# Kernel optimization log

Hardware: AMD Instinct MI355X
Metric: run time of the kernel (lower is better)

## Reference

```python
import jax, jax.numpy as jnp
import numpy as np

C, H_HEADS, L_LEV, M_PTS = 256, 4, 3, 4
TAU0 = 1.0


def _ln(x, g, b, eps=1e-5):
    mu = x.mean(-1, keepdims=True)
    var = ((x - mu) ** 2).mean(-1, keepdims=True)
    return (x - mu) * jax.lax.rsqrt(var + eps) * g + b


def _grid_sample(v, grid):
    """Bilinear grid_sample, padding_mode='zeros', align_corners=True.
    v: [B,C,Hin,Win], grid: [B,N,2] (x,y) in [-1,1] -> [B,N,C]"""
    B, Cc, Hin, Win = v.shape
    x = (grid[..., 0] + 1.0) * 0.5 * (Win - 1)
    y = (grid[..., 1] + 1.0) * 0.5 * (Hin - 1)
    x0 = jnp.floor(x); y0 = jnp.floor(y)
    wx1 = x - x0; wy1 = y - y0
    x0i = x0.astype(jnp.int32); y0i = y0.astype(jnp.int32)
    vflat = v.reshape(B, Cc, Hin * Win).transpose(0, 2, 1)  # [B,HW,C]

    def tap(yi, xi, w):
        valid = ((xi >= 0) & (xi < Win) & (yi >= 0) & (yi < Hin)).astype(v.dtype)
        idx = jnp.clip(yi, 0, Hin - 1) * Win + jnp.clip(xi, 0, Win - 1)  # [B,N]
        g = jax.vmap(lambda vf, i: vf[i])(vflat, idx)  # [B,N,C]
        return g * (w * valid)[..., None]

    return (tap(y0i, x0i, (1 - wy1) * (1 - wx1))
            + tap(y0i, x0i + 1, (1 - wy1) * wx1)
            + tap(y0i + 1, x0i, wy1 * (1 - wx1))
            + tap(y0i + 1, x0i + 1, wy1 * wx1))


def setup_inputs() -> dict:
    key = jax.random.key(0)
    ks = jax.random.split(key, 32)
    B, Hq, Wq = 2, 64, 64
    cins = [256, 512, 1024]
    d = {
        'S':  jax.random.normal(ks[0], (B, C, Hq, Wq), jnp.float32),
        'f0': jax.random.normal(ks[1], (B, cins[0], 64, 64), jnp.float32),
        'f1': jax.random.normal(ks[2], (B, cins[1], 32, 32), jnp.float32),
        'f2': jax.random.normal(ks[3], (B, cins[2], 16, 16), jnp.float32),
        'sim': jax.random.uniform(ks[4], (B, 1, Hq, Wq), jnp.float32),
        # 1x1 conv value projections per level
        'vw0': jax.random.normal(ks[5], (C, cins[0]), jnp.float32) * 0.02,
        'vb0': jnp.zeros((C,), jnp.float32),
        'vw1': jax.random.normal(ks[6], (C, cins[1]), jnp.float32) * 0.02,
        'vb1': jnp.zeros((C,), jnp.float32),
        'vw2': jax.random.normal(ks[7], (C, cins[2]), jnp.float32) * 0.02,
        'vb2': jnp.zeros((C,), jnp.float32),
        'q_w': jax.random.normal(ks[8], (C, C), jnp.float32) * 0.02,
        'q_b': jnp.zeros((C,), jnp.float32),
        # offset/weight predictors (non-zero so sampling is nontrivial)
        'off_w': jax.random.normal(ks[9], (H_HEADS * L_LEV * M_PTS * 2, C), jnp.float32) * 0.01,
        'off_b': jnp.zeros((H_HEADS * L_LEV * M_PTS * 2,), jnp.float32),
        'wgt_w': jax.random.normal(ks[10], (H_HEADS * L_LEV * M_PTS, C), jnp.float32) * 0.02,
        'wgt_b': jnp.zeros((H_HEADS * L_LEV * M_PTS,), jnp.float32),
        'out_w': jax.random.normal(ks[11], (C, H_HEADS * C), jnp.float32) * 0.02,
        'out_b': jnp.zeros((C,), jnp.float32),
        'lnq_g': jnp.ones((C,), jnp.float32), 'lnq_b': jnp.zeros((C,), jnp.float32),
        'lno_g': jnp.ones((C,), jnp.float32), 'lno_b': jnp.zeros((C,), jnp.float32),
        'fc1_w': jax.random.normal(ks[12], (4 * C, C), jnp.float32) * 0.02,
        'fc1_b': jnp.zeros((4 * C,), jnp.float32),
        'fc2_w': jax.random.normal(ks[13], (C, 4 * C), jnp.float32) * 0.02,
        'fc2_b': jnp.zeros((C,), jnp.float32),
    }
    return d


def reference(S, f0, f1, f2, sim, vw0, vb0, vw1, vb1, vw2, vb2, q_w, q_b,
              off_w, off_b, wgt_w, wgt_b, out_w, out_b,
              lnq_g, lnq_b, lno_g, lno_b, fc1_w, fc1_b, fc2_w, fc2_b):
    B, Cc, Hq, Wq = S.shape
    Nq = Hq * Wq
    S_seq = S.reshape(B, Cc, Nq).transpose(0, 2, 1)  # [B,Nq,C]
    Q = _ln(S_seq @ q_w.T + q_b, lnq_g, lnq_b)

    # reference points in [0,1], (x,y)
    ys = jnp.linspace(0.5 / Hq, 1 - 0.5 / Hq, Hq)
    xs = jnp.linspace(0.5 / Wq, 1 - 0.5 / Wq, Wq)
    yy, xx = jnp.meshgrid(ys, xs, indexing='ij')
    ref = jnp.stack([xx, yy], axis=-1).reshape(1, Nq, 2)

    feats = [(f0, vw0, vb0), (f1, vw1, vb1), (f2, vw2, vb2)]
    V = [jnp.einsum('bchw,oc->bohw', f, w) + b[None, :, None, None] for f, w, b in feats]

    off = (Q @ off_w.T + off_b).reshape(B, Nq, H_HEADS, L_LEV, M_PTS, 2)
    wts = (Q @ wgt_w.T + wgt_b).reshape(B, Nq, H_HEADS, L_LEV, M_PTS)

    sim2 = sim[:, 0].reshape(B, Nq, 1)
    tau = TAU0 / (sim2 + 0.001)
    wts = wts / tau.reshape(B, Nq, 1, 1, 1)
    wts = jax.nn.softmax(wts.reshape(B, Nq, H_HEADS, L_LEV * M_PTS), axis=-1)
    wts = wts.reshape(B, Nq, H_HEADS, L_LEV, M_PTS)

    acc = jnp.zeros((B, Nq, H_HEADS, Cc), S.dtype)
    for l in range(L_LEV):
        g01 = ref.reshape(1, Nq, 1, 1, 2) + off[:, :, :, l]  # [B,Nq,H,M,2]
        g = jnp.clip(jnp.tanh(g01 * 2.0 - 1.0), -1.0, 1.0)
        samp = _grid_sample(V[l], g.reshape(B, Nq * H_HEADS * M_PTS, 2))
        samp = samp.reshape(B, Nq, H_HEADS, M_PTS, Cc)
        acc = acc + jnp.einsum('bqhmc,bqhm->bqhc', samp, wts[:, :, :, l])

    Y = acc.reshape(B, Nq, H_HEADS * Cc) @ out_w.T + out_b
    Z = _ln(S_seq + Y, lno_g, lno_b)
    h = jax.nn.gelu(Z @ fc1_w.T + fc1_b, approximate=False)
    Z = Z + (h @ fc2_w.T + fc2_b)
    return Z.transpose(0, 2, 1).reshape(B, Cc, Hq, Wq)
```

## Files before the change

kernel.cpp:

```cpp
#include <hip/hip_runtime.h>
#include <hip/hip_bf16.h>
#include <math.h>

#define NQ 4096
#define CC 256

typedef __attribute__((ext_vector_type(8))) short bfrag;
typedef __attribute__((ext_vector_type(4))) float ffrag;

__device__ inline unsigned short f2bf(float x) {
  __hip_bfloat16 h = __float2bfloat16(x);
  return *reinterpret_cast<unsigned short*>(&h);
}

__device__ inline void gload16(const void* g, void* l) {
  __builtin_amdgcn_global_load_lds(
      (const __attribute__((address_space(1))) void*)g,
      (__attribute__((address_space(3))) void*)l, 16, 0, 0);
}

__device__ void tr64(const float* __restrict__ src,
                     unsigned short* __restrict__ dstb, int Cin, int P,
                     int p0, int c0, int b, float (*t)[73]) {
  int tid = threadIdx.x;
  int rx = tid & 15, ry = tid >> 4;
  const float* Sb = src + (size_t)b * Cin * P + p0 + rx * 4;
  #pragma unroll
  for (int i = 0; i < 4; i++) {
    int r = ry + i * 16;
    float4 v = *(const float4*)(Sb + (size_t)(c0 + r) * P);
    t[r][rx * 4 + 0] = v.x; t[r][rx * 4 + 1] = v.y;
    t[r][rx * 4 + 2] = v.z; t[r][rx * 4 + 3] = v.w;
  }
  __syncthreads();
  size_t ob = (size_t)b * P * Cin;
  #pragma unroll
  for (int i = 0; i < 4; i++) {
    int pr = ry + i * 16;
    float x0 = t[rx * 4 + 0][pr], x1 = t[rx * 4 + 1][pr];
    float x2 = t[rx * 4 + 2][pr], x3 = t[rx * 4 + 3][pr];
    size_t idx = ob + (size_t)(p0 + pr) * Cin + c0 + rx * 4;
    ushort4 u4;
    u4.x = f2bf(x0); u4.y = f2bf(x1); u4.z = f2bf(x2); u4.w = f2bf(x3);
    *(ushort4*)(dstb + idx) = u4;
  }
}

__global__ __launch_bounds__(256)
void prep_all_k(const float* S, const float* f0, const float* f1, const float* f2,
                const float* q_w, const float* off_w, const float* wgt_w,
                const float* vw0, const float* vw1, const float* vw2,
                const float* out_w, const float* fc1_w, const float* fc2_w,
                const float* off_b, const float* wgt_b,
                unsigned short* Sbf,
                unsigned short* Xf0, unsigned short* Xf1, unsigned short* Xf2,
                unsigned short* q_wb, unsigned short* owb,
                unsigned short* vw0b, unsigned short* vw1b, unsigned short* vw2b,
                unsigned short* out_wb, unsigned short* fc1_wb,
                unsigned short* fc2_wb, float* bias144) {
  __shared__ float t[64][73];
  int bid = blockIdx.x;
  if (bid < 512) {
    int l = bid;
    tr64(S, Sbf, 256, 4096, (l & 63) * 64, ((l >> 6) & 3) * 64, l >> 8, t);
  } else if (bid < 1024) {
    int l = bid - 512;
    tr64(f0, Xf0, 256, 4096, (l & 63) * 64, ((l >> 6) & 3) * 64, l >> 8, t);
  } else if (bid < 1280) {
    int l = bid - 1024;
    tr64(f1, Xf1, 512, 1024, (l & 15) * 64, ((l >> 4) & 7) * 64, l >> 7, t);
  } else if (bid < 1408) {
    int l = bid - 1280;
    tr64(f2, Xf2, 1024, 256, (l & 3) * 64, ((l >> 2) & 15) * 64, l >> 6, t);
  } else if (bid < 2688) {
    int i4 = (bid - 1408) * 256 + threadIdx.x;
    const float* src; unsigned short* dst;
    if (i4 < 16384)       { src = q_w;   dst = q_wb; }
    else if (i4 < 32768)  { i4 -= 16384;  src = vw0;   dst = vw0b; }
    else if (i4 < 65536)  { i4 -= 32768;  src = vw1;   dst = vw1b; }
    else if (i4 < 131072) { i4 -= 65536;  src = vw2;   dst = vw2b; }
    else if (i4 < 196608) { i4 -= 131072; src = out_w; dst = out_wb; }
    else if (i4 < 262144) { i4 -= 196608; src = fc1_w; dst = fc1_wb; }
    else                  { i4 -= 262144; src = fc2_w; dst = fc2_wb; }
    float4 v = ((const float4*)src)[i4];
    ushort4 u; u.x = f2bf(v.x); u.y = f2bf(v.y); u.z = f2bf(v.z); u.w = f2bf(v.w);
    ((ushort4*)dst)[i4] = u;
  } else {
    int e = (bid - 2688) * 256 + threadIdx.x;
    float v = (e < 24576) ? off_w[e] : (e < 36864 ? wgt_w[e - 24576] : 0.f);
    owb[e] = f2bf(v);
    if (e < 96) bias144[e] = off_b[e];
    else if (e < 144) bias144[e] = wgt_b[e - 96];
  }
}

template<int BM, int BN, int WM, int WN, int EPI>
__device__ __forceinline__ void gemm_body(
    const unsigned short* __restrict__ A, const unsigned short* __restrict__ B,
    const float* __restrict__ bias, float* __restrict__ outf,
    unsigned short* __restrict__ outb, int N, int Kloop, int lda, int ldb,
    int ldo, const float* __restrict__ Zres, float* __restrict__ outT,
    int m0, int n0, unsigned short* As, unsigned short* Bs) {
  constexpr int MI = BM / (WM * 16), NI = BN / (WN * 16);
  constexpr int TA = BM / 8, TB = BN / 8;
  constexpr int LBM = (BM == 32) ? 5 : (BM == 64) ? 6 : 7;
  constexpr int LBN = (BN == 64) ? 6 : (BN == 128) ? 7 : 8;
  int tid = threadIdx.x, wave = tid >> 6, lane = tid & 63;
  int quad = lane >> 4, l16 = lane & 15;
  int wm = wave / WN, wn = wave % WN;
  const int mbase = wm * (BM / WM), nbase = wn * (BN / WN);

  ffrag acc[MI][NI];
  #pragma unroll
  for (int i = 0; i < MI; i++)
    #pragma unroll
    for (int j = 0; j < NI; j++) acc[i][j] = (ffrag)0.f;

  for (int k0 = 0; k0 < Kloop; k0 += 64) {
    __syncthreads();
    for (int t = wave; t < TA + TB; t += 4) {
      if (t < TA) {
        int s = t * 64 + lane;
        int kc = s >> LBM, r = s & (BM - 1);
        gload16(A + (size_t)(m0 + r) * lda + k0 + kc * 8, (char*)As + t * 1024);
      } else {
        int s = (t - TA) * 64 + lane;
        int kc = s >> LBN, r = s & (BN - 1);
        gload16(B + (size_t)(n0 + r) * ldb + k0 + kc * 8, (char*)Bs + (t - TA) * 1024);
      }
    }
    __syncthreads();
    #pragma unroll
    for (int ks = 0; ks < 2; ks++) {
      bfrag af[MI], bf[NI];
      #pragma unroll
      for (int mi = 0; mi < MI; mi++)
        af[mi] = *(const bfrag*)(As + ((((ks * 4 + quad) << LBM) + mbase + mi * 16 + l16) << 3));
      #pragma unroll
      for (int ni = 0; ni < NI; ni++)
        bf[ni] = *(const bfrag*)(Bs + ((((ks * 4 + quad) << LBN) + nbase + ni * 16 + l16) << 3));
      #pragma unroll
      for (int mi = 0; mi < MI; mi++)
        #pragma unroll
        for (int ni = 0; ni < NI; ni++)
          acc[mi][ni] = __builtin_amdgcn_mfma_f32_16x16x32_bf16(
              af[mi], bf[ni], acc[mi][ni], 0, 0, 0);
    }
  }

  if (EPI == 2) {
    #pragma unroll
    for (int mi = 0; mi < MI; mi++) {
      int mrow = m0 + mbase + mi * 16 + quad * 4;
      int bb = mrow >> 12, q0 = mrow & (NQ - 1);
      #pragma unroll
      for (int ni = 0; ni < NI; ni++) {
        int n = n0 + nbase + ni * 16 + l16;
        float bv = bias[n];
        float4 v;
        v.x = acc[mi][ni][0] + bv + Zres[(size_t)(mrow + 0) * CC + n];
        v.y = acc[mi][ni][1] + bv + Zres[(size_t)(mrow + 1) * CC + n];
        v.z = acc[mi][ni][2] + bv + Zres[(size_t)(mrow + 2) * CC + n];
        v.w = acc[mi][ni][3] + bv + Zres[(size_t)(mrow + 3) * CC + n];
        *(float4*)(outT + ((size_t)(bb * CC + n)) * NQ + q0) = v;
      }
    }
  } else {
    #pragma unroll
    for (int mi = 0; mi < MI; mi++) {
      int mrow = m0 + mbase + mi * 16 + quad * 4;
      #pragma unroll
      for (int ni = 0; ni < NI; ni++) {
        int n = n0 + nbase + ni * 16 + l16;
        if (n < N) {
          float bv = (EPI == 4) ? 0.f : bias[n];
          #pragma unroll
          for (int r = 0; r < 4; r++) {
            float v = acc[mi][ni][r] + bv;
            if (EPI == 1) {
              v = 0.5f * v * (1.f + erff(v * 0.70710678118654752f));
              outb[(size_t)(mrow + r) * ldo + n] = f2bf(v);
            } else if (EPI == 3) {
              outb[(size_t)(mrow + r) * ldo + n] = f2bf(v);
            } else {
              outf[(size_t)(mrow + r) * ldo + n] = v;
            }
          }
        }
      }
    }
  }
}

__device__ __forceinline__ void gemm_ln_q(
    const unsigned short* __restrict__ A, const unsigned short* __restrict__ B,
    const float* __restrict__ bias, unsigned short* __restrict__ outb,
    const float* __restrict__ g, const float* __restrict__ be,
    int m0, char* sm) {
  unsigned short* As = (unsigned short*)sm;
  unsigned short* Bs = (unsigned short*)(sm + 4096);
  float* L = (float*)sm;
  const int K = 256;

  int tid = threadIdx.x, wave = tid >> 6, lane = tid & 63;
  int quad = lane >> 4, l16 = lane & 15;

  ffrag acc[2][4];
  #pragma unroll
  for (int i = 0; i < 2; i++)
    #pragma unroll
    for (int j = 0; j < 4; j++) acc[i][j] = (ffrag)0.f;

  for (int k0 = 0; k0 < K; k0 += 64) {
    __syncthreads();
    for (int t = wave; t < 36; t += 4) {
      if (t < 4) {
        int s = t * 64 + lane;
        int kc = s >> 5, r = s & 31;
        gload16(A + (size_t)(m0 + r) * K + k0 + kc * 8, sm + t * 1024);
      } else {
        int s = (t - 4) * 64 + lane;
        int kc = s >> 8, r = s & 255;
        gload16(B + (size_t)r * K + k0 + kc * 8, sm + 4096 + (t - 4) * 1024);
      }
    }
    __syncthreads();
    #pragma unroll
    for (int ks = 0; ks < 2; ks++) {
      bfrag af[2], bf[4];
      #pragma unroll
      for (int mi = 0; mi < 2; mi++)
        af[mi] = *(const bfrag*)(As + ((((ks * 4 + quad) << 5) + mi * 16 + l16) << 3));
      #pragma unroll
      for (int ni = 0; ni < 4; ni++)
        bf[ni] = *(const bfrag*)(Bs + ((((ks * 4 + quad) << 8) + wave * 64 + ni * 16 + l16) << 3));
      #pragma unroll
      for (int mi = 0; mi < 2; mi++)
        #pragma unroll
        for (int ni = 0; ni < 4; ni++)
          acc[mi][ni] = __builtin_amdgcn_mfma_f32_16x16x32_bf16(
              af[mi], bf[ni], acc[mi][ni], 0, 0, 0);
    }
  }
  __syncthreads();

  #pragma unroll
  for (int mi = 0; mi < 2; mi++) {
    int row = mi * 16 + quad * 4;
    #pragma unroll
    for (int ni = 0; ni < 4; ni++) {
      int col = wave * 64 + ni * 16 + l16;
      float bv = bias[col];
      #pragma unroll
      for (int r = 0; r < 4; r++)
        L[(row + r) * 264 + col] = acc[mi][ni][r] + bv;
    }
  }
  __syncthreads();

  int row = tid >> 3, j = tid & 7;
  int seg = ((j + row) & 7) * 32;
  const float* Lr = L + row * 264 + seg;
  float s1 = 0.f, s2 = 0.f;
  #pragma unroll
  for (int i = 0; i < 8; i++) {
    float4 t4 = *(const float4*)(Lr + i * 4);
    s1 += t4.x + t4.y + t4.z + t4.w;
    s2 += t4.x * t4.x + t4.y * t4.y + t4.z * t4.z + t4.w * t4.w;
  }
  #pragma unroll
  for (int o = 1; o < 8; o <<= 1) {
    s1 += __shfl_xor(s1, o);
    s2 += __shfl_xor(s2, o);
  }
  float mu = s1 * (1.f / 256.f);
  float var = s2 * (1.f / 256.f) - mu * mu;
  float rs = rsqrtf(var + 1e-5f);
  int gm = m0 + row;
  #pragma unroll
  for (int i = 0; i < 8; i++) {
    int col = seg + i * 4;
    float4 t4 = *(const float4*)(Lr + i * 4);
    float4 gg = *(const float4*)(g + col);
    float4 bb4 = *(const float4*)(be + col);
    ushort4 ub;
    ub.x = f2bf((t4.x - mu) * rs * gg.x + bb4.x);
    ub.y = f2bf((t4.y - mu) * rs * gg.y + bb4.y);
    ub.z = f2bf((t4.z - mu) * rs * gg.z + bb4.z);
    ub.w = f2bf((t4.w - mu) * rs * gg.w + bb4.w);
    *(ushort4*)(outb + (size_t)gm * CC + col) = ub;
  }
}

__global__ __launch_bounds__(256)
void qv_k(const unsigned short* Sbf, const unsigned short* q_wb, const float* q_b,
          const float* lnq_g, const float* lnq_b, unsigned short* Qbf,
          const unsigned short* Xf0, const unsigned short* Xf1,
          const unsigned short* Xf2, const unsigned short* vw0b,
          const unsigned short* vw1b, const unsigned short* vw2b,
          const float* vb0, unsigned short* V0b, float* Vp1, float* Vp2) {
  __shared__ __attribute__((aligned(16))) char sm[36864];
  int bid = blockIdx.x;
  unsigned short* As = (unsigned short*)sm;
  unsigned short* Bs = (unsigned short*)(sm + 8192);
  if (bid < 256) {
    gemm_ln_q(Sbf, q_wb, q_b, Qbf, lnq_g, lnq_b, bid * 32, sm);
  } else if (bid < 512) {
    int t = bid - 256;
    gemm_body<64, 128, 2, 2, 3>(Xf0, vw0b, vb0, nullptr, V0b, 256, 256, 256, 256,
                                256, nullptr, nullptr, (t >> 1) * 64, (t & 1) * 128, As, Bs);
  } else if (bid < 640) {
    int l = bid - 512, ks = l >> 6, t = l & 63;
    gemm_body<64, 128, 2, 2, 4>(Xf1 + ks * 256, vw1b + ks * 256, nullptr,
                                Vp1 + (size_t)ks * 524288, nullptr, 256, 256, 512, 512,
                                256, nullptr, nullptr, (t >> 1) * 64, (t & 1) * 128, As, Bs);
  } else {
    int l = bid - 640, ks = l >> 4, t = l & 15;
    gemm_body<64, 128, 2, 2, 4>(Xf2 + ks * 256, vw2b + ks * 256, nullptr,
                                Vp2 + (size_t)ks * 131072, nullptr, 256, 256, 1024, 1024,
                                256, nullptr, nullptr, (t >> 1) * 64, (t & 1) * 128, As, Bs);
  }
}

__global__ __launch_bounds__(256)
void offv_k(const unsigned short* Qbf, const unsigned short* owb,
            const float* bias144, float* offwgt,
            const float* Vp1, const float* Vp2, const float* vb1,
            const float* vb2, unsigned short* V1b, unsigned short* V2b) {
  __shared__ __attribute__((aligned(16))) unsigned short As[4096];
  __shared__ __attribute__((aligned(16))) unsigned short Bs[8192];
  int bid = blockIdx.x;
  if (bid < 256) {
    gemm_body<64, 128, 2, 2, 0>(Qbf, owb, bias144, offwgt, nullptr, 144, 256, 256,
                                256, 144, nullptr, nullptr,
                                (bid >> 1) * 64, (bid & 1) * 128, As, Bs);
  } else if (bid < 768) {
    int e4 = (bid - 256) * 256 + threadIdx.x;
    const float4* P = (const float4*)Vp1;
    float4 a = P[e4], b = P[e4 + 131072];
    float4 bb = *(const float4*)(vb1 + ((e4 << 2) & 255));
    ushort4 u;
    u.x = f2bf(a.x + b.x + bb.x); u.y = f2bf(a.y + b.y + bb.y);
    u.z = f2bf(a.z + b.z + bb.z); u.w = f2bf(a.w + b.w + bb.w);
    ((ushort4*)V1b)[e4] = u;
  } else {
    int e4 = (bid - 768) * 256 + threadIdx.x;
    const float4* P = (const float4*)Vp2;
    float4 a = P[e4], b = P[e4 + 32768], c = P[e4 + 65536], d = P[e4 + 98304];
    float4 bb = *(const float4*)(vb2 + ((e4 << 2) & 255));
    ushort4 u;
    u.x = f2bf(a.x + b.x + c.x + d.x + bb.x);
    u.y = f2bf(a.y + b.y + c.y + d.y + bb.y);
    u.z = f2bf(a.z + b.z + c.z + d.z + bb.z);
    u.w = f2bf(a.w + b.w + c.w + d.w + bb.w);
    ((ushort4*)V2b)[e4] = u;
  }
}

__global__ __launch_bounds__(256)
void outA_k(const unsigned short* accbf, const unsigned short* out_wb, float* Op) {
  __shared__ __attribute__((aligned(16))) char sm[36864];
  int ks = blockIdx.y;
  gemm_body<32, 256, 1, 4, 4>(accbf + ks * 256, out_wb + ks * 256, nullptr,
                              Op + (size_t)ks * 2097152, nullptr, 256, 256, 1024,
                              1024, 256, nullptr, nullptr, blockIdx.x * 32, 0,
                              (unsigned short*)sm, (unsigned short*)(sm + 4096));
}

__global__ __launch_bounds__(256)
void outB_k(const float* __restrict__ Op, const float* __restrict__ S,
            const float* __restrict__ out_b, const float* __restrict__ g,
            const float* __restrict__ be, float* __restrict__ Zf,
            unsigned short* __restrict__ Zbf) {
  __shared__ float Ls[16][264];
  int q0 = blockIdx.x * 16;
  int b = q0 >> 12, qq = q0 & (NQ - 1);
  int t = threadIdx.x;
  {
    int cs = t >> 2, j = (t & 3) * 4;
    #pragma unroll
    for (int c0 = 0; c0 < 256; c0 += 64) {
      float4 sv = *(const float4*)(S + (((size_t)(b * 256 + c0 + cs)) << 12) + qq + j);
      Ls[j + 0][c0 + cs] = sv.x; Ls[j + 1][c0 + cs] = sv.y;
      Ls[j + 2][c0 + cs] = sv.z; Ls[j + 3][c0 + cs] = sv.w;
    }
  }
  __syncthreads();
  int c = t;
  float bv = out_b[c];
  float val[16];
  #pragma unroll
  for (int r = 0; r < 16; r++) {
    size_t idx = (size_t)(q0 + r) * 256 + c;
    val[r] = Op[idx] + Op[idx + 2097152] + Op[idx + 4194304] + Op[idx + 6291456]
           + bv + Ls[r][c];
  }
  __syncthreads();
  #pragma unroll
  for (int r = 0; r < 16; r++) Ls[r][c] = val[r];
  __syncthreads();
  int row = t >> 4, lg = t & 15;
  const float* Lr = &Ls[row][lg * 16];
  float s1 = 0.f, s2 = 0.f;
  #pragma unroll
  for (int i = 0; i < 4; i++) {
    float4 t4 = *(const float4*)(Lr + i * 4);
    s1 += t4.x + t4.y + t4.z + t4.w;
    s2 += t4.x * t4.x + t4.y * t4.y + t4.z * t4.z + t4.w * t4.w;
  }
  #pragma unroll
  for (int o = 1; o < 16; o <<= 1) {
    s1 += __shfl_xor(s1, o);
    s2 += __shfl_xor(s2, o);
  }
  float mu = s1 * (1.f / 256.f);
  float var = s2 * (1.f / 256.f) - mu * mu;
  float rs = rsqrtf(var + 1e-5f);
  int gm = q0 + row;
  #pragma unroll
  for (int i = 0; i < 4; i++) {
    int col = lg * 16 + i * 4;
    float4 t4 = *(const float4*)(Lr + i * 4);
    float4 gg = *(const float4*)(g + col);
    float4 bb4 = *(const float4*)(be + col);
    float4 y;
    y.x = (t4.x - mu) * rs * gg.x + bb4.x;
    y.y = (t4.y - mu) * rs * gg.y + bb4.y;
    y.z = (t4.z - mu) * rs * gg.z + bb4.z;
    y.w = (t4.w - mu) * rs * gg.w + bb4.w;
    *(float4*)(Zf + (size_t)gm * CC + col) = y;
    ushort4 ub;
    ub.x = f2bf(y.x); ub.y = f2bf(y.y); ub.z = f2bf(y.z); ub.w = f2bf(y.w);
    *(ushort4*)(Zbf + (size_t)gm * CC + col) = ub;
  }
}

__global__ __launch_bounds__(256)
void fc1_k(const unsigned short* Zbf, const unsigned short* fc1_wb,
           const float* fc1_b, unsigned short* hbf) {
  __shared__ __attribute__((aligned(16))) unsigned short As[4096];
  __shared__ __attribute__((aligned(16))) unsigned short Bs[8192];
  gemm_body<64, 128, 2, 2, 1>(Zbf, fc1_wb, fc1_b, nullptr, hbf, 1024, 256, 256,
                              256, 1024, nullptr, nullptr,
                              blockIdx.y * 64, blockIdx.x * 128, As, Bs);
}

__global__ __launch_bounds__(256)
void fc2_k(const unsigned short* hbf, const unsigned short* fc2_wb,
           const float* fc2_b, const float* Z, float* outp) {
  __shared__ __attribute__((aligned(16))) unsigned short As[4096];
  __shared__ __attribute__((aligned(16))) unsigned short Bs[4096];
  gemm_body<64, 64, 2, 2, 2>(hbf, fc2_wb, fc2_b, nullptr, nullptr, 256, 1024,
                             1024, 1024, 256, Z, outp,
                             blockIdx.y * 64, blockIdx.x * 64, As, Bs);
}

__global__ __launch_bounds__(256)
void sample_k(const float* __restrict__ ow, const float* __restrict__ sim,
              const unsigned short* __restrict__ V0, const unsigned short* __restrict__ V1,
              const unsigned short* __restrict__ V2, unsigned short* __restrict__ acc) {
  int bn = blockIdx.x;
  int q = ((bn & 7) << 10) | (bn >> 3);
  int b = q >> 12, n = q & (NQ - 1);
  int tid = threadIdx.x, head = tid >> 6, lane = tid & 63;
  int half = lane >> 5, l32 = lane & 31;

  __shared__ float s_w[48];
  __shared__ int   s_xy[48][2];
  __shared__ float s_f[48][2];
  __shared__ uint2 s_ow[192];

  if (tid < 48) {
    int hh = tid / 12, pt = tid % 12, l = pt >> 2, mm = pt & 3;
    int oidx = (hh * 3 + l) * 4 + mm;
    float offx = ow[(size_t)q * 144 + oidx * 2 + 0];
    float offy = ow[(size_t)q * 144 + oidx * 2 + 1];
    float refx = ((n & 63) + 0.5f) * (1.f / 64.f);
    float refy = ((n >> 6) + 0.5f) * (1.f / 64.f);
    float gx = tanhf((refx + offx) * 2.f - 1.f);
    float gy = tanhf((refy + offy) * 2.f - 1.f);
    gx = fminf(1.f, fmaxf(-1.f, gx));
    gy = fminf(1.f, fmaxf(-1.f, gy));
    int Wl = 64 >> l;
    float x = (gx + 1.f) * 0.5f * (float)(Wl - 1);
    float y = (gy + 1.f) * 0.5f * (float)(Wl - 1);
    float x0 = floorf(x), y0 = floorf(y);
    s_xy[tid][0] = (int)x0;
    s_xy[tid][1] = (int)y0;
    s_f[tid][0] = x - x0;
    s_f[tid][1] = y - y0;
    s_w[tid] = ow[(size_t)q * 144 + 96 + oidx] * (sim[q] + 0.001f);
  }
  __syncthreads();
  if (tid < 4) {
    float mx = -1e30f;
    #pragma unroll
    for (int i = 0; i < 12; i++) mx = fmaxf(mx, s_w[tid * 12 + i]);
    float e[12], ssum = 0.f;
    #pragma unroll
    for (int i = 0; i < 12; i++) { e[i] = expf(s_w[tid * 12 + i] - mx); ssum += e[i]; }
    float inv = 1.f / ssum;
    #pragma unroll
    for (int i = 0; i < 12; i++) s_w[tid * 12 + i] = e[i] * inv;
  }
  __syncthreads();
  if (tid < 192) {
    int s = tid >> 2, tap = tid & 3;
    int l = (s % 12) >> 2;
    int Wl = 64 >> l;
    int X = s_xy[s][0] + (tap & 1), Y = s_xy[s][1] + (tap >> 1);
    bool valid = (X >= 0 && X < Wl && Y >= 0 && Y < Wl);
    float wx = (tap & 1) ? s_f[s][0] : 1.f - s_f[s][0];
    float wy = (tap >> 1) ? s_f[s][1] : 1.f - s_f[s][1];
    float twt = valid ? s_w[s] * wx * wy : 0.f;
    int Xc = min(max(X, 0), Wl - 1), Yc = min(max(Y, 0), Wl - 1);
    s_ow[tid].x = (unsigned)((Yc * Wl + Xc) << 8);
    s_ow[tid].y = __float_as_uint(twt);
  }
  __syncthreads();

  const unsigned short* B0 = V0 + (size_t)b * 4096 * CC;
  const unsigned short* B1 = V1 + (size_t)b * 1024 * CC;
  const unsigned short* B2 = V2 + (size_t)b * 256 * CC;
  int ch8 = l32 * 8;
  float a0 = 0.f, a1 = 0.f, a2 = 0.f, a3 = 0.f;
  float a4 = 0.f, a5 = 0.f, a6 = 0.f, a7 = 0.f;
  #pragma unroll
  for (int it = 0; it < 24; it++) {
    const unsigned short* base = (it < 8) ? B0 : (it < 16) ? B1 : B2;
    uint2 owv = s_ow[head * 48 + it * 2 + half];
    float w = __uint_as_float(owv.y);
    const uint4 u = *(const uint4*)(base + owv.x + ch8);
    a0 = fmaf(w, __uint_as_float(u.x << 16), a0);
    a1 = fmaf(w, __uint_as_float(u.x & 0xffff0000u), a1);
    a2 = fmaf(w, __uint_as_float(u.y << 16), a2);
    a3 = fmaf(w, __uint_as_float(u.y & 0xffff0000u), a3);
    a4 = fmaf(w, __uint_as_float(u.z << 16), a4);
    a5 = fmaf(w, __uint_as_float(u.z & 0xffff0000u), a5);
    a6 = fmaf(w, __uint_as_float(u.w << 16), a6);
    a7 = fmaf(w, __uint_as_float(u.w & 0xffff0000u), a7);
  }
  a0 += __shfl_xor(a0, 32); a1 += __shfl_xor(a1, 32);
  a2 += __shfl_xor(a2, 32); a3 += __shfl_xor(a3, 32);
  a4 += __shfl_xor(a4, 32); a5 += __shfl_xor(a5, 32);
  a6 += __shfl_xor(a6, 32); a7 += __shfl_xor(a7, 32);
  if (half == 0) {
    uint4 r;
    r.x = (unsigned)f2bf(a0) | ((unsigned)f2bf(a1) << 16);
    r.y = (unsigned)f2bf(a2) | ((unsigned)f2bf(a3) << 16);
    r.z = (unsigned)f2bf(a4) | ((unsigned)f2bf(a5) << 16);
    r.w = (unsigned)f2bf(a6) | ((unsigned)f2bf(a7) << 16);
    *(uint4*)(acc + (size_t)q * 1024 + head * CC + ch8) = r;
  }
}

extern "C" void kernel_launch(void* const* d_in, const int* in_sizes, int n_in,
                              void* d_out, int out_size, void* d_ws, size_t ws_size,
                              hipStream_t stream) {
  const float* S     = (const float*)d_in[0];
  const float* f0    = (const float*)d_in[1];
  const float* f1    = (const float*)d_in[2];
  const float* f2    = (const float*)d_in[3];
  const float* sim   = (const float*)d_in[4];
  const float* vw0   = (const float*)d_in[5];
  const float* vb0   = (const float*)d_in[6];
  const float* vw1   = (const float*)d_in[7];
  const float* vb1   = (const float*)d_in[8];
  const float* vw2   = (const float*)d_in[9];
  const float* vb2   = (const float*)d_in[10];
  const float* q_w   = (const float*)d_in[11];
  const float* q_b   = (const float*)d_in[12];
  const float* off_w = (const float*)d_in[13];
  const float* off_b = (const float*)d_in[14];
  const float* wgt_w = (const float*)d_in[15];
  const float* wgt_b = (const float*)d_in[16];
  const float* out_w = (const float*)d_in[17];
  const float* out_b = (const float*)d_in[18];
  const float* lnq_g = (const float*)d_in[19];
  const float* lnq_b = (const float*)d_in[20];
  const float* lno_g = (const float*)d_in[21];
  const float* lno_b = (const float*)d_in[22];
  const float* fc1_w = (const float*)d_in[23];
  const float* fc1_b = (const float*)d_in[24];
  const float* fc2_w = (const float*)d_in[25];
  const float* fc2_b = (const float*)d_in[26];

  char* p = (char*)d_ws;
  float* Z      = (float*)p; p += 8388608;
  float* offwgt = (float*)p; p += 4718592;
  float* bias144 = (float*)p; p += 1024;
  float* Pp     = (float*)p; p += 33554432;
  float* Vp1    = (float*)p; p += 4194304;
  float* Vp2    = (float*)p; p += 2097152;
  unsigned short* Sbf   = (unsigned short*)p; p += 4194304;
  unsigned short* Qbf   = (unsigned short*)p; p += 4194304;
  unsigned short* accbf = (unsigned short*)p; p += 16777216;
  unsigned short* V0b   = (unsigned short*)p; p += 4194304;
  unsigned short* V1b   = (unsigned short*)p; p += 1048576;
  unsigned short* V2b   = (unsigned short*)p; p += 262144;
  unsigned short* q_wb   = (unsigned short*)p; p += 131072;
  unsigned short* owb    = (unsigned short*)p; p += 131072;
  unsigned short* vw0b   = (unsigned short*)p; p += 131072;
  unsigned short* vw1b   = (unsigned short*)p; p += 262144;
  unsigned short* vw2b   = (unsigned short*)p; p += 524288;
  unsigned short* out_wb = (unsigned short*)p; p += 524288;
  unsigned short* fc1_wb = (unsigned short*)p; p += 524288;
  unsigned short* fc2_wb = (unsigned short*)p; p += 524288;

  unsigned short* Xf0 = accbf;
  unsigned short* Xf1 = accbf + 2097152;
  unsigned short* Xf2 = accbf + 3145728;
  unsigned short* Zbf = Qbf;
  unsigned short* hbf = accbf;
  float* outp = (float*)d_out;

  prep_all_k<<<2944, 256, 0, stream>>>(S, f0, f1, f2, q_w, off_w, wgt_w,
      vw0, vw1, vw2, out_w, fc1_w, fc2_w, off_b, wgt_b,
      Sbf, Xf0, Xf1, Xf2, q_wb, owb, vw0b, vw1b, vw2b, out_wb,
      fc1_wb, fc2_wb, bias144);

  qv_k<<<704, 256, 0, stream>>>(Sbf, q_wb, q_b, lnq_g, lnq_b, Qbf,
      Xf0, Xf1, Xf2, vw0b, vw1b, vw2b, vb0, V0b, Vp1, Vp2);

  offv_k<<<896, 256, 0, stream>>>(Qbf, owb, bias144, offwgt,
      Vp1, Vp2, vb1, vb2, V1b, V2b);

  sample_k<<<8192, 256, 0, stream>>>(offwgt, sim, V0b, V1b, V2b, accbf);

  outA_k<<<dim3(256, 4), 256, 0, stream>>>(accbf, out_wb, Pp);

  outB_k<<<512, 256, 0, stream>>>(Pp, S, out_b, lno_g, lno_b, Z, Zbf);

  fc1_k<<<dim3(8, 128), 256, 0, stream>>>(Zbf, fc1_wb, fc1_b, hbf);

  fc2_k<<<dim3(4, 128), 256, 0, stream>>>(hbf, fc2_wb, fc2_b, Z, outp);
}
```

Baseline: 269.1 us.

## Drop fp32 Z buffer, halve outA split-K, widen fc1/offset GEMM tiles

Stops writing the fp32 LayerNorm output Z and makes the fc2 residual read the bf16 Zbf copy instead, which removes an 8 MB write plus read. The out-projection split-K drops from 4 to 2 slices, so there are fewer fp32 partials to write and reduce in outB. The fc1 and offset/weight GEMMs use 64x256 tiles instead of 64x128, giving more reuse of the A tile. The risks are lower residual precision from using bf16 Z, and less parallelism in outA and fc1.

```diff
diff --git a/kernel.cpp b/kernel.cpp
--- a/kernel.cpp
+++ b/kernel.cpp
@@ -11,6 +11,10 @@
 __device__ inline unsigned short f2bf(float x) {
   __hip_bfloat16 h = __float2bfloat16(x);
   return *reinterpret_cast<unsigned short*>(&h);
+}
+
+__device__ inline float bf2f(unsigned short u) {
+  return __uint_as_float(((unsigned)u) << 16);
 }
 
 __device__ inline void gload16(const void* g, void* l) {
@@ -99,7 +103,7 @@
     const unsigned short* __restrict__ A, const unsigned short* __restrict__ B,
     const float* __restrict__ bias, float* __restrict__ outf,
     unsigned short* __restrict__ outb, int N, int Kloop, int lda, int ldb,
-    int ldo, const float* __restrict__ Zres, float* __restrict__ outT,
+    int ldo, const unsigned short* __restrict__ Zres, float* __restrict__ outT,
     int m0, int n0, unsigned short* As, unsigned short* Bs) {
   constexpr int MI = BM / (WM * 16), NI = BN / (WN * 16);
   constexpr int TA = BM / 8, TB = BN / 8;
@@ -158,10 +162,10 @@
         int n = n0 + nbase + ni * 16 + l16;
         float bv = bias[n];
         float4 v;
-        v.x = acc[mi][ni][0] + bv + Zres[(size_t)(mrow + 0) * CC + n];
-        v.y = acc[mi][ni][1] + bv + Zres[(size_t)(mrow + 1) * CC + n];
-        v.z = acc[mi][ni][2] + bv + Zres[(size_t)(mrow + 2) * CC + n];
-        v.w = acc[mi][ni][3] + bv + Zres[(size_t)(mrow + 3) * CC + n];
+        v.x = acc[mi][ni][0] + bv + bf2f(Zres[(size_t)(mrow + 0) * CC + n]);
+        v.y = acc[mi][ni][1] + bv + bf2f(Zres[(size_t)(mrow + 1) * CC + n]);
+        v.z = acc[mi][ni][2] + bv + bf2f(Zres[(size_t)(mrow + 2) * CC + n]);
+        v.w = acc[mi][ni][3] + bv + bf2f(Zres[(size_t)(mrow + 3) * CC + n]);
         *(float4*)(outT + ((size_t)(bb * CC + n)) * NQ + q0) = v;
       }
     }
@@ -328,14 +332,13 @@
             const float* Vp1, const float* Vp2, const float* vb1,
             const float* vb2, unsigned short* V1b, unsigned short* V2b) {
   __shared__ __attribute__((aligned(16))) unsigned short As[4096];
-  __shared__ __attribute__((aligned(16))) unsigned short Bs[8192];
+  __shared__ __attribute__((aligned(16))) unsigned short Bs[16384];
   int bid = blockIdx.x;
-  if (bid < 256) {
-    gemm_body<64, 128, 2, 2, 0>(Qbf, owb, bias144, offwgt, nullptr, 144, 256, 256,
-                                256, 144, nullptr, nullptr,
-                                (bid >> 1) * 64, (bid & 1) * 128, As, Bs);
-  } else if (bid < 768) {
-    int e4 = (bid - 256) * 256 + threadIdx.x;
+  if (bid < 128) {
+    gemm_body<64, 256, 2, 2, 0>(Qbf, owb, bias144, offwgt, nullptr, 144, 256, 256,
+                                256, 144, nullptr, nullptr, bid * 64, 0, As, Bs);
+  } else if (bid < 640) {
+    int e4 = (bid - 128) * 256 + threadIdx.x;
     const float4* P = (const float4*)Vp1;
     float4 a = P[e4], b = P[e4 + 131072];
     float4 bb = *(const float4*)(vb1 + ((e4 << 2) & 255));
@@ -344,7 +347,7 @@
     u.z = f2bf(a.z + b.z + bb.z); u.w = f2bf(a.w + b.w + bb.w);
     ((ushort4*)V1b)[e4] = u;
   } else {
-    int e4 = (bid - 768) * 256 + threadIdx.x;
+    int e4 = (bid - 640) * 256 + threadIdx.x;
     const float4* P = (const float4*)Vp2;
     float4 a = P[e4], b = P[e4 + 32768], c = P[e4 + 65536], d = P[e4 + 98304];
     float4 bb = *(const float4*)(vb2 + ((e4 << 2) & 255));
@@ -361,8 +364,8 @@
 void outA_k(const unsigned short* accbf, const unsigned short* out_wb, float* Op) {
   __shared__ __attribute__((aligned(16))) char sm[36864];
   int ks = blockIdx.y;
-  gemm_body<32, 256, 1, 4, 4>(accbf + ks * 256, out_wb + ks * 256, nullptr,
-                              Op + (size_t)ks * 2097152, nullptr, 256, 256, 1024,
+  gemm_body<32, 256, 1, 4, 4>(accbf + ks * 512, out_wb + ks * 512, nullptr,
+                              Op + (size_t)ks * 2097152, nullptr, 256, 512, 1024,
                               1024, 256, nullptr, nullptr, blockIdx.x * 32, 0,
                               (unsigned short*)sm, (unsigned short*)(sm + 4096));
 }
@@ -370,8 +373,7 @@
 __global__ __launch_bounds__(256)
 void outB_k(const float* __restrict__ Op, const float* __restrict__ S,
             const float* __restrict__ out_b, const float* __restrict__ g,
-            const float* __restrict__ be, float* __restrict__ Zf,
-            unsigned short* __restrict__ Zbf) {
+            const float* __restrict__ be, unsigned short* __restrict__ Zbf) {
   __shared__ float Ls[16][264];
   int q0 = blockIdx.x * 16;
   int b = q0 >> 12, qq = q0 & (NQ - 1);
@@ -392,8 +394,7 @@
   #pragma unroll
   for (int r = 0; r < 16; r++) {
     size_t idx = (size_t)(q0 + r) * 256 + c;
-    val[r] = Op[idx] + Op[idx + 2097152] + Op[idx + 4194304] + Op[idx + 6291456]
-           + bv + Ls[r][c];
+    val[r] = Op[idx] + Op[idx + 2097152] + bv + Ls[r][c];
   }
   __syncthreads();
   #pragma unroll
@@ -423,14 +424,11 @@
     float4 t4 = *(const float4*)(Lr + i * 4);
     float4 gg = *(const float4*)(g + col);
     float4 bb4 = *(const float4*)(be + col);
-    float4 y;
-    y.x = (t4.x - mu) * rs * gg.x + bb4.x;
-    y.y = (t4.y - mu) * rs * gg.y + bb4.y;
-    y.z = (t4.z - mu) * rs * gg.z + bb4.z;
-    y.w = (t4.w - mu) * rs * gg.w + bb4.w;
-    *(float4*)(Zf + (size_t)gm * CC + col) = y;
     ushort4 ub;
-    ub.x = f2bf(y.x); ub.y = f2bf(y.y); ub.z = f2bf(y.z); ub.w = f2bf(y.w);
+    ub.x = f2bf((t4.x - mu) * rs * gg.x + bb4.x);
+    ub.y = f2bf((t4.y - mu) * rs * gg.y + bb4.y);
+    ub.z = f2bf((t4.z - mu) * rs * gg.z + bb4.z);
+    ub.w = f2bf((t4.w - mu) * rs * gg.w + bb4.w);
     *(ushort4*)(Zbf + (size_t)gm * CC + col) = ub;
   }
 }
@@ -439,19 +437,19 @@
 void fc1_k(const unsigned short* Zbf, const unsigned short* fc1_wb,
            const float* fc1_b, unsigned short* hbf) {
   __shared__ __attribute__((aligned(16))) unsigned short As[4096];
-  __shared__ __attribute__((aligned(16))) unsigned short Bs[8192];
-  gemm_body<64, 128, 2, 2, 1>(Zbf, fc1_wb, fc1_b, nullptr, hbf, 1024, 256, 256,
+  __shared__ __attribute__((aligned(16))) unsigned short Bs[16384];
+  gemm_body<64, 256, 2, 2, 1>(Zbf, fc1_wb, fc1_b, nullptr, hbf, 1024, 256, 256,
                               256, 1024, nullptr, nullptr,
-                              blockIdx.y * 64, blockIdx.x * 128, As, Bs);
+                              blockIdx.y * 64, blockIdx.x * 256, As, Bs);
 }
 
 __global__ __launch_bounds__(256)
 void fc2_k(const unsigned short* hbf, const unsigned short* fc2_wb,
-           const float* fc2_b, const float* Z, float* outp) {
+           const float* fc2_b, const unsigned short* Zbf, float* outp) {
   __shared__ __attribute__((aligned(16))) unsigned short As[4096];
   __shared__ __attribute__((aligned(16))) unsigned short Bs[4096];
   gemm_body<64, 64, 2, 2, 2>(hbf, fc2_wb, fc2_b, nullptr, nullptr, 256, 1024,
-                             1024, 1024, 256, Z, outp,
+                             1024, 1024, 256, Zbf, outp,
                              blockIdx.y * 64, blockIdx.x * 64, As, Bs);
 }
 
@@ -586,10 +584,9 @@
   const float* fc2_b = (const float*)d_in[26];
 
   char* p = (char*)d_ws;
-  float* Z      = (float*)p; p += 8388608;
   float* offwgt = (float*)p; p += 4718592;
   float* bias144 = (float*)p; p += 1024;
-  float* Pp     = (float*)p; p += 33554432;
+  float* Pp     = (float*)p; p += 16777216;
   float* Vp1    = (float*)p; p += 4194304;
   float* Vp2    = (float*)p; p += 2097152;
   unsigned short* Sbf   = (unsigned short*)p; p += 4194304;
@@ -622,16 +619,16 @@
   qv_k<<<704, 256, 0, stream>>>(Sbf, q_wb, q_b, lnq_g, lnq_b, Qbf,
       Xf0, Xf1, Xf2, vw0b, vw1b, vw2b, vb0, V0b, Vp1, Vp2);
 
-  offv_k<<<896, 256, 0, stream>>>(Qbf, owb, bias144, offwgt,
+  offv_k<<<768, 256, 0, stream>>>(Qbf, owb, bias144, offwgt,
       Vp1, Vp2, vb1, vb2, V1b, V2b);
 
   sample_k<<<8192, 256, 0, stream>>>(offwgt, sim, V0b, V1b, V2b, accbf);
 
-  outA_k<<<dim3(256, 4), 256, 0, stream>>>(accbf, out_wb, Pp);
-
-  outB_k<<<512, 256, 0, stream>>>(Pp, S, out_b, lno_g, lno_b, Z, Zbf);
-
-  fc1_k<<<dim3(8, 128), 256, 0, stream>>>(Zbf, fc1_wb, fc1_b, hbf);
-
-  fc2_k<<<dim3(4, 128), 256, 0, stream>>>(hbf, fc2_wb, fc2_b, Z, outp);
-}
+  outA_k<<<dim3(256, 2), 256, 0, stream>>>(accbf, out_wb, Pp);
+
+  outB_k<<<512, 256, 0, stream>>>(Pp, S, out_b, lno_g, lno_b, Zbf);
+
+  fc1_k<<<dim3(4, 128), 256, 0, stream>>>(Zbf, fc1_wb, fc1_b, hbf);
+
+  fc2_k<<<dim3(4, 128), 256, 0, stream>>>(hbf, fc2_wb, fc2_b, Zbf, outp);
+}
```

Result: faster. 263.8 us (-2.0%).
